# Performance work log

Measured on AMD Instinct MI355X. Metric: run time of the kernel, lower is better.

Reference implementation:

```python
import jax, jax.numpy as jnp
import numpy as np
from jax.scipy.special import logsumexp

F = 200000   # numFactors
V = 100000   # numVars
S = 5        # state_dimensions (binary vars -> factor tables are (2,)*S)
E = 1000000  # number of factor-to-variable edges


def setup_inputs() -> dict:
    key = jax.random.key(0)
    ks = jax.random.split(key, 8)
    shape_f = (F,) + (2,) * S
    return {
        "factor_beliefs": jax.random.normal(ks[0], shape_f, jnp.float32),
        "var_beliefs": jax.random.normal(ks[1], (V, 2), jnp.float32),
        "factor_potentials": jax.random.normal(ks[2], shape_f, jnp.float32),
        "prv_varToFactor_messages": jax.random.normal(ks[3], (E, 2), jnp.float32),
        "prv_factorToVar_messages": jax.random.normal(ks[4], (E, 2), jnp.float32),
        "f2v_factor_idx": jax.random.randint(ks[5], (E,), 0, F),
        "f2v_var_idx": jax.random.randint(ks[6], (E,), 0, V),
        "edge_var_idx": jax.random.randint(ks[7], (E,), 0, S),
    }


def _bp_iteration(factor_beliefs, var_beliefs, factor_potentials,
                  prv_v2f, prv_f2v, f_idx, v_idx, ev_idx):
    nF = factor_beliefs.shape[0]
    nV = var_beliefs.shape[0]
    nS = factor_beliefs.ndim - 1  # state_dimensions

    # ---- message_factorToVar ----
    mapped_f = factor_beliefs[f_idx]  # [E, 2,...,2] gather along edges
    # logsumexp over all factor axes except each candidate axis d -> [E, S, 2]
    lse_per_axis = jnp.stack(
        [logsumexp(mapped_f, axis=tuple(a for a in range(1, nS + 1) if a != d + 1))
         for d in range(nS)], axis=1)
    # pick per-edge the axis this edge's variable occupies -> [E, 2]
    marg = jnp.take_along_axis(lse_per_axis, ev_idx[:, None, None], axis=1)[:, 0, :]
    f2v_msgs = marg - jnp.where(jnp.isneginf(prv_v2f), 0.0, prv_v2f)

    # ---- var beliefs: scatter-add over edges, then per-var normalization ----
    var_b = jax.ops.segment_sum(f2v_msgs, v_idx, num_segments=nV)
    var_b = var_b - logsumexp(var_b, axis=1, keepdims=True)

    # ---- message_varToFactor ----
    mapped_v = var_b[v_idx]  # [E, 2]
    v2f_msgs = mapped_v - jnp.where(jnp.isneginf(prv_f2v), 0.0, prv_f2v)

    # ---- expand each [2] message along its per-edge factor axis -> [E, 2^S] ----
    # expanded[e, i0..i_{S-1}] = msg[e, i_{ev_idx[e]}]
    idx_grid = jnp.indices((2,) * nS).reshape(nS, -1)  # [S, 2^S] coord along each axis
    sel = idx_grid[ev_idx]                              # [E, 2^S]
    expanded = jnp.take_along_axis(v2f_msgs, sel, axis=1)  # [E, 2^S]

    # ---- factor beliefs: scatter-add, add potentials, normalize per factor ----
    fb = jax.ops.segment_sum(expanded, f_idx, num_segments=nF)
    fb = fb.reshape((nF,) + (2,) * nS) + factor_potentials
    fb_flat = fb.reshape(nF, -1)
    fb = (fb_flat - logsumexp(fb_flat, axis=1, keepdims=True)).reshape(fb.shape)

    return var_b, fb, f2v_msgs, v2f_msgs


def reference(factor_beliefs, var_beliefs, factor_potentials,
              prv_varToFactor_messages, prv_factorToVar_messages,
              f2v_factor_idx, f2v_var_idx, edge_var_idx):
    # Returns (new var_beliefs, new factor_beliefs,
    #          prv_factorToVar_messages', prv_varToFactor_messages')
    return _bp_iteration(factor_beliefs, var_beliefs, factor_potentials,
                         prv_varToFactor_messages, prv_factorToVar_messages,
                         f2v_factor_idx, f2v_var_idx, edge_var_idx)
```

## Files before the change

### kernel.cpp

```cpp
#include <hip/hip_runtime.h>
#include <math.h>

__global__ void __launch_bounds__(256) k1_f2v(
    const float* __restrict__ fbel,
    const float* __restrict__ pv2f,
    const int*   __restrict__ fidx,
    const int*   __restrict__ vidx,
    const int*   __restrict__ evidx,
    float* __restrict__ f2v_out,
    float* __restrict__ vacc,
    int E)
{
    int e = blockIdx.x * 256 + threadIdx.x;
    if (e >= E) return;
    int f   = fidx[e];
    int bit = 4 - evidx[e];

    const float4* tab = reinterpret_cast<const float4*>(fbel + (size_t)f * 32);
    float v[32];
#pragma unroll
    for (int q = 0; q < 8; ++q) {
        float4 t = tab[q];
        v[q*4+0] = t.x; v[q*4+1] = t.y; v[q*4+2] = t.z; v[q*4+3] = t.w;
    }

    float m0 = -INFINITY, m1 = -INFINITY;
#pragma unroll
    for (int j = 0; j < 32; ++j) {
        bool hi = (j >> bit) & 1;
        if (hi) m1 = fmaxf(m1, v[j]); else m0 = fmaxf(m0, v[j]);
    }
    float s0 = 0.f, s1 = 0.f;
#pragma unroll
    for (int j = 0; j < 32; ++j) {
        bool hi = (j >> bit) & 1;
        float ex = __expf(v[j] - (hi ? m1 : m0));
        if (hi) s1 += ex; else s0 += ex;
    }
    float marg0 = m0 + __logf(s0);
    float marg1 = m1 + __logf(s1);

    float p0 = pv2f[2*e],   p1 = pv2f[2*e+1];
    p0 = (p0 == -INFINITY) ? 0.f : p0;
    p1 = (p1 == -INFINITY) ? 0.f : p1;
    float r0 = marg0 - p0, r1 = marg1 - p1;

    f2v_out[2*e]   = r0;
    f2v_out[2*e+1] = r1;

    int vi = vidx[e];
    atomicAdd(&vacc[2*vi],   r0);
    atomicAdd(&vacc[2*vi+1], r1);
}

__global__ void __launch_bounds__(256) k2_varnorm(float* __restrict__ vb, int V)
{
    int v = blockIdx.x * 256 + threadIdx.x;
    if (v >= V) return;
    float a0 = vb[2*v], a1 = vb[2*v+1];
    float m = fmaxf(a0, a1);
    float l = m + __logf(__expf(a0 - m) + __expf(a1 - m));
    vb[2*v]   = a0 - l;
    vb[2*v+1] = a1 - l;
}

__global__ void __launch_bounds__(256) k3_v2f(
    const float* __restrict__ vb,
    const float* __restrict__ pf2v,
    const int*   __restrict__ fidx,
    const int*   __restrict__ vidx,
    const int*   __restrict__ evidx,
    float* __restrict__ v2f_out,
    float* __restrict__ facc,
    int E)
{
    int e = blockIdx.x * 256 + threadIdx.x;
    if (e >= E) return;
    int vi = vidx[e];
    float b0 = vb[2*vi], b1 = vb[2*vi+1];
    float p0 = pf2v[2*e], p1 = pf2v[2*e+1];
    p0 = (p0 == -INFINITY) ? 0.f : p0;
    p1 = (p1 == -INFINITY) ? 0.f : p1;
    float r0 = b0 - p0, r1 = b1 - p1;

    v2f_out[2*e]   = r0;
    v2f_out[2*e+1] = r1;

    int f = fidx[e], d = evidx[e];
    atomicAdd(&facc[(size_t)f*10 + d*2    ], r0);
    atomicAdd(&facc[(size_t)f*10 + d*2 + 1], r1);
}

__global__ void __launch_bounds__(256) k4_fb(
    const float* __restrict__ facc,
    const float* __restrict__ pot,
    float* __restrict__ fb_out,
    int F)
{
    int f = blockIdx.x * 256 + threadIdx.x;
    if (f >= F) return;

    float a[10];
#pragma unroll
    for (int i = 0; i < 10; ++i) a[i] = facc[(size_t)f*10 + i];

    float t[32];
    const float4* pp = reinterpret_cast<const float4*>(pot + (size_t)f * 32);
#pragma unroll
    for (int q = 0; q < 8; ++q) {
        float4 x = pp[q];
        t[q*4+0] = x.x; t[q*4+1] = x.y; t[q*4+2] = x.z; t[q*4+3] = x.w;
    }

    float m = -INFINITY;
#pragma unroll
    for (int j = 0; j < 32; ++j) {
        float s = t[j];
#pragma unroll
        for (int d = 0; d < 5; ++d) s += a[d*2 + ((j >> (4 - d)) & 1)];
        t[j] = s;
        m = fmaxf(m, s);
    }
    float sum = 0.f;
#pragma unroll
    for (int j = 0; j < 32; ++j) sum += __expf(t[j] - m);
    float l = m + __logf(sum);

    float4* out = reinterpret_cast<float4*>(fb_out + (size_t)f * 32);
#pragma unroll
    for (int q = 0; q < 8; ++q) {
        float4 x;
        x.x = t[q*4+0] - l; x.y = t[q*4+1] - l;
        x.z = t[q*4+2] - l; x.w = t[q*4+3] - l;
        out[q] = x;
    }
}

extern "C" void kernel_launch(void* const* d_in, const int* in_sizes, int n_in,
                              void* d_out, int out_size, void* d_ws, size_t ws_size,
                              hipStream_t stream)
{
    const float* fbel  = (const float*)d_in[0];
    const float* pot   = (const float*)d_in[2];
    const float* pv2f  = (const float*)d_in[3];
    const float* pf2v  = (const float*)d_in[4];
    const int*   fidx  = (const int*)d_in[5];
    const int*   vidx  = (const int*)d_in[6];
    const int*   evidx = (const int*)d_in[7];

    const int E  = in_sizes[5];
    const int F_ = in_sizes[0] / 32;
    const int V_ = in_sizes[1] / 2;

    float* out     = (float*)d_out;
    float* var_out = out;
    float* fb_out  = out + (size_t)V_ * 2;
    float* f2v_out = fb_out + (size_t)F_ * 32;
    float* v2f_out = f2v_out + (size_t)E * 2;

    float* facc = (float*)d_ws;

    hipMemsetAsync(var_out, 0, (size_t)V_ * 2 * sizeof(float), stream);
    hipMemsetAsync(facc,    0, (size_t)F_ * 10 * sizeof(float), stream);

    k1_f2v    <<<dim3((E  + 255) / 256), dim3(256), 0, stream>>>(
        fbel, pv2f, fidx, vidx, evidx, f2v_out, var_out, E);
    k2_varnorm<<<dim3((V_ + 255) / 256), dim3(256), 0, stream>>>(var_out, V_);
    k3_v2f    <<<dim3((E  + 255) / 256), dim3(256), 0, stream>>>(
        var_out, pf2v, fidx, vidx, evidx, v2f_out, facc, E);
    k4_fb     <<<dim3((F_ + 255) / 256), dim3(256), 0, stream>>>(
        facc, pot, fb_out, F_);
}
```

Baseline: 339.3 us.

## Precompute per-factor per-axis marginals once instead of per edge

Adds a kernel that computes all ten per-axis logsumexp marginals of each factor table once, stored in the v2f output region as scratch. The edge kernel then gathers an 8-byte float2 instead of a 128-byte table and no longer recomputes 32 exponentials per edge. This removes roughly five times redundant gather traffic and transcendental work, at the cost of an extra launch and an F*10 write and read. Using one global max per factor instead of a per-slice max is slightly less robust numerically. Loads and stores in the edge kernels are also vectorised to float2.

```diff
diff --git a/kernel.cpp b/kernel.cpp
--- a/kernel.cpp
+++ b/kernel.cpp
@@ -1,8 +1,43 @@
 #include <hip/hip_runtime.h>
 #include <math.h>
 
+__global__ void __launch_bounds__(256) k0_flse(
+    const float* __restrict__ fbel,
+    float* __restrict__ flse,
+    int F)
+{
+    int f = blockIdx.x * 256 + threadIdx.x;
+    if (f >= F) return;
+
+    const float4* tab = reinterpret_cast<const float4*>(fbel + (size_t)f * 32);
+    float v[32];
+#pragma unroll
+    for (int q = 0; q < 8; ++q) {
+        float4 t = tab[q];
+        v[q*4+0] = t.x; v[q*4+1] = t.y; v[q*4+2] = t.z; v[q*4+3] = t.w;
+    }
+
+    float m = v[0];
+#pragma unroll
+    for (int j = 1; j < 32; ++j) m = fmaxf(m, v[j]);
+
+    float s[10];
+#pragma unroll
+    for (int i = 0; i < 10; ++i) s[i] = 0.f;
+#pragma unroll
+    for (int j = 0; j < 32; ++j) {
+        float ex = __expf(v[j] - m);
+#pragma unroll
+        for (int d = 0; d < 5; ++d) s[d*2 + ((j >> (4 - d)) & 1)] += ex;
+    }
+
+    float* o = flse + (size_t)f * 10;
+#pragma unroll
+    for (int i = 0; i < 10; ++i) o[i] = m + __logf(s[i]);
+}
+
 __global__ void __launch_bounds__(256) k1_f2v(
-    const float* __restrict__ fbel,
+    const float* __restrict__ flse,
     const float* __restrict__ pv2f,
     const int*   __restrict__ fidx,
     const int*   __restrict__ vidx,
@@ -13,40 +48,15 @@
 {
     int e = blockIdx.x * 256 + threadIdx.x;
     if (e >= E) return;
-    int f   = fidx[e];
-    int bit = 4 - evidx[e];
+    int f = fidx[e], d = evidx[e];
 
-    const float4* tab = reinterpret_cast<const float4*>(fbel + (size_t)f * 32);
-    float v[32];
-#pragma unroll
-    for (int q = 0; q < 8; ++q) {
-        float4 t = tab[q];
-        v[q*4+0] = t.x; v[q*4+1] = t.y; v[q*4+2] = t.z; v[q*4+3] = t.w;
-    }
+    float2 lse = *reinterpret_cast<const float2*>(flse + (size_t)f * 10 + d * 2);
+    float2 p   = *reinterpret_cast<const float2*>(pv2f + 2 * (size_t)e);
+    float p0 = (p.x == -INFINITY) ? 0.f : p.x;
+    float p1 = (p.y == -INFINITY) ? 0.f : p.y;
+    float r0 = lse.x - p0, r1 = lse.y - p1;
 
-    float m0 = -INFINITY, m1 = -INFINITY;
-#pragma unroll
-    for (int j = 0; j < 32; ++j) {
-        bool hi = (j >> bit) & 1;
-        if (hi) m1 = fmaxf(m1, v[j]); else m0 = fmaxf(m0, v[j]);
-    }
-    float s0 = 0.f, s1 = 0.f;
-#pragma unroll
-    for (int j = 0; j < 32; ++j) {
-        bool hi = (j >> bit) & 1;
-        float ex = __expf(v[j] - (hi ? m1 : m0));
-        if (hi) s1 += ex; else s0 += ex;
-    }
-    float marg0 = m0 + __logf(s0);
-    float marg1 = m1 + __logf(s1);
-
-    float p0 = pv2f[2*e],   p1 = pv2f[2*e+1];
-    p0 = (p0 == -INFINITY) ? 0.f : p0;
-    p1 = (p1 == -INFINITY) ? 0.f : p1;
-    float r0 = marg0 - p0, r1 = marg1 - p1;
-
-    f2v_out[2*e]   = r0;
-    f2v_out[2*e+1] = r1;
+    *reinterpret_cast<float2*>(f2v_out + 2 * (size_t)e) = make_float2(r0, r1);
 
     int vi = vidx[e];
     atomicAdd(&vacc[2*vi],   r0);
@@ -77,14 +87,13 @@
     int e = blockIdx.x * 256 + threadIdx.x;
     if (e >= E) return;
     int vi = vidx[e];
-    float b0 = vb[2*vi], b1 = vb[2*vi+1];
-    float p0 = pf2v[2*e], p1 = pf2v[2*e+1];
-    p0 = (p0 == -INFINITY) ? 0.f : p0;
-    p1 = (p1 == -INFINITY) ? 0.f : p1;
-    float r0 = b0 - p0, r1 = b1 - p1;
+    float2 b = *reinterpret_cast<const float2*>(vb + 2 * (size_t)vi);
+    float2 p = *reinterpret_cast<const float2*>(pf2v + 2 * (size_t)e);
+    float p0 = (p.x == -INFINITY) ? 0.f : p.x;
+    float p1 = (p.y == -INFINITY) ? 0.f : p.y;
+    float r0 = b.x - p0, r1 = b.y - p1;
 
-    v2f_out[2*e]   = r0;
-    v2f_out[2*e+1] = r1;
+    *reinterpret_cast<float2*>(v2f_out + 2 * (size_t)e) = make_float2(r0, r1);
 
     int f = fidx[e], d = evidx[e];
     atomicAdd(&facc[(size_t)f*10 + d*2    ], r0);
@@ -158,13 +167,15 @@
     float* f2v_out = fb_out + (size_t)F_ * 32;
     float* v2f_out = f2v_out + (size_t)E * 2;
 
+    float* flse = v2f_out;
     float* facc = (float*)d_ws;
 
     hipMemsetAsync(var_out, 0, (size_t)V_ * 2 * sizeof(float), stream);
     hipMemsetAsync(facc,    0, (size_t)F_ * 10 * sizeof(float), stream);
 
+    k0_flse   <<<dim3((F_ + 255) / 256), dim3(256), 0, stream>>>(fbel, flse, F_);
     k1_f2v    <<<dim3((E  + 255) / 256), dim3(256), 0, stream>>>(
-        fbel, pv2f, fidx, vidx, evidx, f2v_out, var_out, E);
+        flse, pv2f, fidx, vidx, evidx, f2v_out, var_out, E);
     k2_varnorm<<<dim3((V_ + 255) / 256), dim3(256), 0, stream>>>(var_out, V_);
     k3_v2f    <<<dim3((E  + 255) / 256), dim3(256), 0, stream>>>(
         var_out, pf2v, fidx, vidx, evidx, v2f_out, facc, E);
```

Result: slower. 347.8 us (+2.5%).
